# Kernel tuning notes

Hardware: AMD Instinct MI355X
Metric: run time of the kernel (lower is better)

Reference implementation:

```python
import jax, jax.numpy as jnp
import numpy as np

K = 2  # top-k slots from init kwargs


def setup_inputs() -> dict:
    key = jax.random.key(0)
    ks = jax.random.split(key, 6)
    B, T, d, E, dff = 2, 2048, 512, 8, 2048
    x = jax.random.normal(ks[0], (B, T, d), dtype=jnp.float32)
    Wg = jax.random.normal(ks[1], (d, E), dtype=jnp.float32) * 0.02
    W1 = jax.random.normal(ks[2], (E, d, dff), dtype=jnp.float32) * 0.02
    b1 = jnp.zeros((E, dff), dtype=jnp.float32)
    W2 = jax.random.normal(ks[3], (E, dff, d), dtype=jnp.float32) * 0.02
    b2 = jnp.zeros((E, d), dtype=jnp.float32)
    return {"x": x, "Wg": Wg, "W1": W1, "b1": b1, "W2": W2, "b2": b2}


def reference(x, Wg, W1, b1, W2, b2):
    # Gate: softmax over experts, top-k probs renormalized. Note: in the
    # original code the per-expert gather/scatter masks partition the tokens,
    # so dispatched_input == x * p_i (full weighted input), and ALL experts'
    # MLPs are applied to it and summed (tf.add_n). We reproduce that math.
    logits = jnp.einsum('btd,de->bte', x, Wg)          # [B,T,E]
    probs = jax.nn.softmax(logits, axis=-1)
    top_p, _top_i = jax.lax.top_k(probs, K)            # [B,T,K]
    top_p = top_p / jnp.sum(top_p, axis=-1, keepdims=True)
    b2_sum = jnp.sum(b2, axis=0)                        # sum of all experts' output biases
    out = jnp.zeros_like(x)
    for i in range(K):  # small fixed loop over top-k slots
        w_in = x * top_p[..., i:i + 1]                  # [B,T,d]
        # every expert runs on the full weighted input (faithful to source)
        h = jax.nn.gelu(
            jnp.einsum('btd,edf->ebtf', w_in, W1) + b1[:, None, None, :],
            approximate=False)                           # [E,B,T,dff]
        out = out + jnp.einsum('ebtf,efd->btd', h, W2) + b2_sum
    return out
```

## Files before the change

kernel.cpp:

```cpp
#include <hip/hip_runtime.h>
#include <hip/hip_bf16.h>
#include <cstdint>

#define TOKENS 4096
#define DMODEL 512
#define NEXP 8
#define DFF 2048

typedef short s16x8 __attribute__((ext_vector_type(8)));
typedef short s16x4 __attribute__((ext_vector_type(4)));
typedef float f32x4 __attribute__((ext_vector_type(4)));

__device__ __forceinline__ float bf2f(short h) {
    unsigned int u = ((unsigned int)(unsigned short)h) << 16;
    return __uint_as_float(u);
}
__device__ __forceinline__ short f2bf(float f) {
    unsigned int u = __float_as_uint(f);
    u += 0x7fffu + ((u >> 16) & 1u);
    return (short)(u >> 16);
}
__device__ __forceinline__ float gelu_f(float x) {
    float x2 = x * x;
    float z2 = x * fmaf(x2, 0.07135481627260025f, 1.5957691216057308f);
    float ex = __expf(z2);
    float r = __builtin_amdgcn_rcpf(1.0f + ex);
    return x - x * r;
}
__device__ __forceinline__ void gload_lds16(const void* g, void* l) {
    __builtin_amdgcn_global_load_lds((const __attribute__((address_space(1))) void*)g,
                                     (__attribute__((address_space(3))) void*)l, 16, 0, 0);
}

__global__ void gate_cvt_kernel(const float* __restrict__ x, const float* __restrict__ Wg,
                                float* __restrict__ s0, float* __restrict__ s1,
                                short* __restrict__ xb) {
    int wave = threadIdx.x >> 6;
    int lane = threadIdx.x & 63;
    int t = blockIdx.x * 4 + wave;
    const float* xr = x + (size_t)t * DMODEL + lane * 8;
    float4 xa = *(const float4*)(xr);
    float4 xv2 = *(const float4*)(xr + 4);
    float xv[8] = {xa.x, xa.y, xa.z, xa.w, xv2.x, xv2.y, xv2.z, xv2.w};
    s16x8 v;
#pragma unroll
    for (int j = 0; j < 8; j++) v[j] = f2bf(xv[j]);
    *(s16x8*)&xb[(size_t)t * DMODEL + lane * 8] = v;

    float lg[8];
#pragma unroll
    for (int e = 0; e < 8; e++) lg[e] = 0.f;
#pragma unroll
    for (int j = 0; j < 8; j++) {
        const float4* wr = (const float4*)(Wg + (size_t)(lane * 8 + j) * NEXP);
        float4 wa = wr[0], wb = wr[1];
        lg[0] = fmaf(xv[j], wa.x, lg[0]);
        lg[1] = fmaf(xv[j], wa.y, lg[1]);
        lg[2] = fmaf(xv[j], wa.z, lg[2]);
        lg[3] = fmaf(xv[j], wa.w, lg[3]);
        lg[4] = fmaf(xv[j], wb.x, lg[4]);
        lg[5] = fmaf(xv[j], wb.y, lg[5]);
        lg[6] = fmaf(xv[j], wb.z, lg[6]);
        lg[7] = fmaf(xv[j], wb.w, lg[7]);
    }
#pragma unroll
    for (int off = 32; off > 0; off >>= 1) {
#pragma unroll
        for (int e = 0; e < 8; e++) lg[e] += __shfl_xor(lg[e], off, 64);
    }
    float l0 = lg[0]; int i0 = 0;
#pragma unroll
    for (int e = 1; e < 8; e++) { if (lg[e] > l0) { l0 = lg[e]; i0 = e; } }
    float l1 = -3.4e38f;
#pragma unroll
    for (int e = 0; e < 8; e++) { if (e != i0 && lg[e] > l1) l1 = lg[e]; }
    float p1 = expf(l1 - l0);
    float sa = 1.0f / (1.0f + p1);
    if (lane == 0) { s0[t] = sa; s1[t] = p1 * sa; }
}

__global__ void transpose_cvt_kernel(const float* __restrict__ in, short* __restrict__ out,
                                     int R, int C) {
    __shared__ float t[64][33];
    int b = blockIdx.z;
    const float* ip = in + (size_t)b * R * C;
    short* op = out + (size_t)b * R * C;
    int c0 = blockIdx.x * 64, r0 = blockIdx.y * 32;
    int tid = threadIdx.x;
    int lr = tid >> 3, lc8 = (tid & 7) * 8;
    const float* src = &ip[(size_t)(r0 + lr) * C + c0 + lc8];
    float4 v0 = *(const float4*)src;
    float4 v1 = *(const float4*)(src + 4);
    t[lc8 + 0][lr] = v0.x; t[lc8 + 1][lr] = v0.y; t[lc8 + 2][lr] = v0.z; t[lc8 + 3][lr] = v0.w;
    t[lc8 + 4][lr] = v1.x; t[lc8 + 5][lr] = v1.y; t[lc8 + 6][lr] = v1.z; t[lc8 + 7][lr] = v1.w;
    __syncthreads();
    int sc = tid >> 2, sk = (tid & 3) * 8;
    s16x8 o;
#pragma unroll
    for (int j = 0; j < 8; j++) o[j] = f2bf(t[sc][sk + j]);
    *(s16x8*)&op[(size_t)(c0 + sc) * R + r0 + sk] = o;
}

__launch_bounds__(256, 2)
__global__ void gemm1_kernel(const short* __restrict__ xb, const short* __restrict__ w1t,
                             const float* __restrict__ s0v, const float* __restrict__ s1v,
                             const float* __restrict__ b1, short* __restrict__ H) {
    __shared__ short Al[128 * 64];
    __shared__ short Bl[128 * 64];
    __shared__ float ls0[128], ls1[128], lb1[128];
    int d = blockIdx.x;
    int e = d & 7;
    int tno = d >> 3;
    int n0 = (tno & 15) * 128;
    int m0 = (tno >> 4) * 128;
    const short* A = xb;
    const short* B = w1t + (size_t)e * DFF * DMODEL;
    short* Ho = H + (size_t)e * TOKENS * DFF;

    int tid = threadIdx.x;
    int lane = tid & 63;
    int w = tid >> 6;
    int m_off = (w >> 1) * 64;
    int n_off = (w & 1) * 64;

    if (tid < 128) {
        ls0[tid] = s0v[m0 + tid];
        ls1[tid] = s1v[m0 + tid];
        lb1[tid] = b1[(size_t)e * DFF + n0 + tid];
    }

    int srow = lane >> 3;
    int schunk = (lane & 7) ^ srow;
    int q = lane >> 4;

    f32x4 acc[4][4];
#pragma unroll
    for (int mi = 0; mi < 4; mi++)
#pragma unroll
        for (int ni = 0; ni < 4; ni++) acc[mi][ni] = (f32x4){0.f, 0.f, 0.f, 0.f};

    for (int k0 = 0; k0 < DMODEL; k0 += 64) {
#pragma unroll
        for (int c = 0; c < 4; c++) {
            int seg = c * 4 + w;
            gload_lds16(&A[(size_t)(m0 + seg * 8 + srow) * DMODEL + k0 + schunk * 8],
                        &Al[seg * 512]);
            gload_lds16(&B[(size_t)(n0 + seg * 8 + srow) * DMODEL + k0 + schunk * 8],
                        &Bl[seg * 512]);
        }
        __syncthreads();
#pragma unroll
        for (int ks = 0; ks < 2; ks++) {
            s16x8 af[4], bfr[4];
#pragma unroll
            for (int mi = 0; mi < 4; mi++) {
                int r = m_off + mi * 16 + (lane & 15);
                int cp = (ks * 4 + q) ^ (r & 7);
                af[mi] = *(const s16x8*)&Al[r * 64 + cp * 8];
            }
#pragma unroll
            for (int ni = 0; ni < 4; ni++) {
                int r = n_off + ni * 16 + (lane & 15);
                int cp = (ks * 4 + q) ^ (r & 7);
                bfr[ni] = *(const s16x8*)&Bl[r * 64 + cp * 8];
            }
#pragma unroll
            for (int mi = 0; mi < 4; mi++)
#pragma unroll
                for (int ni = 0; ni < 4; ni++)
                    acc[mi][ni] = __builtin_amdgcn_mfma_f32_16x16x32_bf16(af[mi], bfr[ni], acc[mi][ni], 0, 0, 0);
        }
        __syncthreads();
    }
#pragma unroll
    for (int mi = 0; mi < 4; mi++) {
        int rl = m_off + mi * 16 + (lane >> 4) * 4;
        float sa4[4], sb4[4];
#pragma unroll
        for (int r = 0; r < 4; r++) { sa4[r] = ls0[rl + r]; sb4[r] = ls1[rl + r]; }
#pragma unroll
        for (int ni = 0; ni < 4; ni++) {
            int cl = n_off + ni * 16 + (lane & 15);
            float bb = lb1[cl];
#pragma unroll
            for (int r = 0; r < 4; r++) {
                float a = acc[mi][ni][r];
                float h = gelu_f(fmaf(sa4[r], a, bb)) + gelu_f(fmaf(sb4[r], a, bb));
                Ho[(size_t)(m0 + rl + r) * DFF + n0 + cl] = f2bf(h);
            }
        }
    }
}

__launch_bounds__(512, 4)
__global__ void gemm2_kernel(const short* __restrict__ H, const short* __restrict__ w2t,
                             float* __restrict__ part) {
    __shared__ short Al[64 * 32];
    __shared__ short Bl[512 * 32];
    int d = blockIdx.x;
    int e = d & 7;
    int m0 = (d >> 3) * 64;
    const short* A = H + (size_t)e * TOKENS * DFF;
    const short* B = w2t + (size_t)e * DMODEL * DFF;
    float* Pe = part + (size_t)e * TOKENS * DMODEL;

    int tid = threadIdx.x;
    int lane = tid & 63;
    int w = tid >> 6;
    int n_off = w * 64;
    int q = lane >> 4;

    int srow = lane >> 2;
    int schunk = (lane & 3) ^ ((lane >> 3) & 3);

    f32x4 acc[4][4];
#pragma unroll
    for (int mi = 0; mi < 4; mi++)
#pragma unroll
        for (int ni = 0; ni < 4; ni++) acc[mi][ni] = (f32x4){0.f, 0.f, 0.f, 0.f};

    for (int f0 = 0; f0 < DFF; f0 += 32) {
#pragma unroll
        for (int c = 0; c < 4; c++) {
            int seg = c * 8 + w;
            gload_lds16(&B[(size_t)(seg * 16 + srow) * DFF + f0 + schunk * 8],
                        &Bl[seg * 512]);
        }
        if (w < 4) {
            gload_lds16(&A[(size_t)(m0 + w * 16 + srow) * DFF + f0 + schunk * 8],
                        &Al[w * 512]);
        }
        __syncthreads();
        {
            s16x8 af[4];
#pragma unroll
            for (int mi = 0; mi < 4; mi++) {
                int r = mi * 16 + (lane & 15);
                int cp = q ^ ((r >> 1) & 3);
                af[mi] = *(const s16x8*)&Al[r * 32 + cp * 8];
            }
#pragma unroll
            for (int ni = 0; ni < 4; ni++) {
                int r = n_off + ni * 16 + (lane & 15);
                int cp = q ^ ((r >> 1) & 3);
                s16x8 bfr = *(const s16x8*)&Bl[r * 32 + cp * 8];
#pragma unroll
                for (int mi = 0; mi < 4; mi++)
                    acc[mi][ni] = __builtin_amdgcn_mfma_f32_16x16x32_bf16(af[mi], bfr, acc[mi][ni], 0, 0, 0);
            }
        }
        __syncthreads();
    }

#pragma unroll
    for (int mi = 0; mi < 4; mi++)
#pragma unroll
        for (int ni = 0; ni < 4; ni++) {
            int row = m0 + mi * 16 + (lane >> 4) * 4;
            int col = n_off + ni * 16 + (lane & 15);
#pragma unroll
            for (int r = 0; r < 4; r++)
                Pe[(size_t)(row + r) * DMODEL + col] = acc[mi][ni][r];
        }
}

__global__ void reduce_kernel(const float* __restrict__ part, const float* __restrict__ b2,
                              float* __restrict__ out) {
    int i = (blockIdx.x * 256 + threadIdx.x) * 4;
    if (i >= TOKENS * DMODEL) return;
    int n = i & (DMODEL - 1);
    float4 s = {0.f, 0.f, 0.f, 0.f};
    float4 bs = {0.f, 0.f, 0.f, 0.f};
#pragma unroll
    for (int e = 0; e < 8; e++) {
        float4 p = *(const float4*)&part[(size_t)e * TOKENS * DMODEL + i];
        s.x += p.x; s.y += p.y; s.z += p.z; s.w += p.w;
        float4 b = *(const float4*)&b2[(size_t)e * DMODEL + n];
        bs.x += b.x; bs.y += b.y; bs.z += b.z; bs.w += b.w;
    }
    s.x += 2.f * bs.x; s.y += 2.f * bs.y; s.z += 2.f * bs.z; s.w += 2.f * bs.w;
    *(float4*)&out[i] = s;
}

extern "C" void kernel_launch(void* const* d_in, const int* in_sizes, int n_in,
                              void* d_out, int out_size, void* d_ws, size_t ws_size,
                              hipStream_t stream) {
    const float* x  = (const float*)d_in[0];
    const float* Wg = (const float*)d_in[1];
    const float* W1 = (const float*)d_in[2];
    const float* b1 = (const float*)d_in[3];
    const float* W2 = (const float*)d_in[4];
    const float* b2 = (const float*)d_in[5];
    float* out = (float*)d_out;

    char* ws = (char*)d_ws;
    float* s0  = (float*)(ws);
    float* s1  = (float*)(ws + 16384);
    short* xb  = (short*)(ws + 32768);
    short* w1t = (short*)(ws + 32768 + 4194304);
    short* w2t = (short*)(ws + 32768 + 4194304 + 16777216);
    short* Hb  = (short*)(ws + 32768 + 4194304 + 2ull * 16777216);
    float* part= (float*)(ws + 32768 + 4194304 + 2ull * 16777216 + 134217728);

    hipLaunchKernelGGL(gate_cvt_kernel, dim3(1024), dim3(256), 0, stream, x, Wg, s0, s1, xb);
    hipLaunchKernelGGL(transpose_cvt_kernel, dim3(32, 16, 8), dim3(256), 0, stream, W1, w1t, 512, 2048);
    hipLaunchKernelGGL(transpose_cvt_kernel, dim3(8, 64, 8), dim3(256), 0, stream, W2, w2t, 2048, 512);
    hipLaunchKernelGGL(gemm1_kernel, dim3(4096), dim3(256), 0, stream, xb, w1t, s0, s1, b1, Hb);
    hipLaunchKernelGGL(gemm2_kernel, dim3(512), dim3(512), 0, stream, Hb, w2t, part);
    hipLaunchKernelGGL(reduce_kernel, dim3(2048), dim3(256), 0, stream, part, b2, out);
}
```

Baseline: 238.4 us.

## Retile gemm2 to 128x128 output tiles with K=64 steps and 256-thread blocks

Changes gemm2 from 64x512 tiles with 512 threads and K=32 steps to 128x128 tiles with 256 threads (2x2 warps of 64x64) and K=64 steps, launching 1024 blocks instead of 512. Each K step now stages 16 KB each of A and B in LDS with a new XOR swizzle, halving the number of barriers per output tile and balancing A/B reuse. In exchange, B tiles are reloaded by the four N-tile blocks sharing each M range, and the larger LDS footprint may lower occupancy.

```diff
diff --git a/kernel.cpp b/kernel.cpp
--- a/kernel.cpp
+++ b/kernel.cpp
@@ -192,14 +192,16 @@
     }
 }
 
-__launch_bounds__(512, 4)
+__launch_bounds__(256, 2)
 __global__ void gemm2_kernel(const short* __restrict__ H, const short* __restrict__ w2t,
                              float* __restrict__ part) {
-    __shared__ short Al[64 * 32];
-    __shared__ short Bl[512 * 32];
+    __shared__ short Al[128 * 64];
+    __shared__ short Bl[128 * 64];
     int d = blockIdx.x;
     int e = d & 7;
-    int m0 = (d >> 3) * 64;
+    int tno = d >> 3;
+    int n0 = (tno & 3) * 128;
+    int m0 = (tno >> 2) * 128;
     const short* A = H + (size_t)e * TOKENS * DFF;
     const short* B = w2t + (size_t)e * DMODEL * DFF;
     float* Pe = part + (size_t)e * TOKENS * DMODEL;
@@ -207,47 +209,49 @@
     int tid = threadIdx.x;
     int lane = tid & 63;
     int w = tid >> 6;
-    int n_off = w * 64;
+    int m_off = (w >> 1) * 64;
+    int n_off = (w & 1) * 64;
+
+    int srow = lane >> 3;
+    int schunk = (lane & 7) ^ srow;
     int q = lane >> 4;
 
-    int srow = lane >> 2;
-    int schunk = (lane & 3) ^ ((lane >> 3) & 3);
-
     f32x4 acc[4][4];
 #pragma unroll
     for (int mi = 0; mi < 4; mi++)
 #pragma unroll
         for (int ni = 0; ni < 4; ni++) acc[mi][ni] = (f32x4){0.f, 0.f, 0.f, 0.f};
 
-    for (int f0 = 0; f0 < DFF; f0 += 32) {
+    for (int k0 = 0; k0 < DFF; k0 += 64) {
 #pragma unroll
         for (int c = 0; c < 4; c++) {
-            int seg = c * 8 + w;
-            gload_lds16(&B[(size_t)(seg * 16 + srow) * DFF + f0 + schunk * 8],
+            int seg = c * 4 + w;
+            gload_lds16(&A[(size_t)(m0 + seg * 8 + srow) * DFF + k0 + schunk * 8],
+                        &Al[seg * 512]);
+            gload_lds16(&B[(size_t)(n0 + seg * 8 + srow) * DFF + k0 + schunk * 8],
                         &Bl[seg * 512]);
         }
-        if (w < 4) {
-            gload_lds16(&A[(size_t)(m0 + w * 16 + srow) * DFF + f0 + schunk * 8],
-                        &Al[w * 512]);
-        }
         __syncthreads();
-        {
-            s16x8 af[4];
+#pragma unroll
+        for (int ks = 0; ks < 2; ks++) {
+            s16x8 af[4], bfr[4];
 #pragma unroll
             for (int mi = 0; mi < 4; mi++) {
-                int r = mi * 16 + (lane & 15);
-                int cp = q ^ ((r >> 1) & 3);
-                af[mi] = *(const s16x8*)&Al[r * 32 + cp * 8];
+                int r = m_off + mi * 16 + (lane & 15);
+                int cp = (ks * 4 + q) ^ (r & 7);
+                af[mi] = *(const s16x8*)&Al[r * 64 + cp * 8];
             }
 #pragma unroll
             for (int ni = 0; ni < 4; ni++) {
                 int r = n_off + ni * 16 + (lane & 15);
-                int cp = q ^ ((r >> 1) & 3);
-                s16x8 bfr = *(const s16x8*)&Bl[r * 32 + cp * 8];
-#pragma unroll
-                for (int mi = 0; mi < 4; mi++)
-                    acc[mi][ni] = __builtin_amdgcn_mfma_f32_16x16x32_bf16(af[mi], bfr, acc[mi][ni], 0, 0, 0);
-            }
+                int cp = (ks * 4 + q) ^ (r & 7);
+                bfr[ni] = *(const s16x8*)&Bl[r * 64 + cp * 8];
+            }
+#pragma unroll
+            for (int mi = 0; mi < 4; mi++)
+#pragma unroll
+                for (int ni = 0; ni < 4; ni++)
+                    acc[mi][ni] = __builtin_amdgcn_mfma_f32_16x16x32_bf16(af[mi], bfr[ni], acc[mi][ni], 0, 0, 0);
         }
         __syncthreads();
     }
@@ -256,8 +260,8 @@
     for (int mi = 0; mi < 4; mi++)
 #pragma unroll
         for (int ni = 0; ni < 4; ni++) {
-            int row = m0 + mi * 16 + (lane >> 4) * 4;
-            int col = n_off + ni * 16 + (lane & 15);
+            int row = m0 + m_off + mi * 16 + (lane >> 4) * 4;
+            int col = n0 + n_off + ni * 16 + (lane & 15);
 #pragma unroll
             for (int r = 0; r < 4; r++)
                 Pe[(size_t)(row + r) * DMODEL + col] = acc[mi][ni][r];
@@ -306,6 +310,6 @@
     hipLaunchKernelGGL(transpose_cvt_kernel, dim3(32, 16, 8), dim3(256), 0, stream, W1, w1t, 512, 2048);
     hipLaunchKernelGGL(transpose_cvt_kernel, dim3(8, 64, 8), dim3(256), 0, stream, W2, w2t, 2048, 512);
     hipLaunchKernelGGL(gemm1_kernel, dim3(4096), dim3(256), 0, stream, xb, w1t, s0, s1, b1, Hb);
-    hipLaunchKernelGGL(gemm2_kernel, dim3(512), dim3(512), 0, stream, Hb, w2t, part);
+    hipLaunchKernelGGL(gemm2_kernel, dim3(1024), dim3(256), 0, stream, Hb, w2t, part);
     hipLaunchKernelGGL(reduce_kernel, dim3(2048), dim3(256), 0, stream, part, b2, out);
 }
```

New measurement: 210.4 us. -11.7%, faster.
